# Optimization experiments

Measured on AMD Instinct MI355X. Metric: run time of the kernel, lower is better.

Reference implementation:

```python
import jax, jax.numpy as jnp
import numpy as np

N = 100000
E = 1600000
D = 128


def setup_inputs() -> dict:
    key = jax.random.key(0)
    ks = jax.random.split(key, 9)
    s = 1.0 / np.sqrt(D)
    return {
        "x": jax.random.normal(ks[0], (N, D), dtype=jnp.float32),
        "edge_index": jax.random.randint(ks[1], (2, E), 0, N, dtype=jnp.int64),
        # SAGEConv layer 1: lin_l (neighbor path, with bias), lin_r (root path, no bias)
        "Wl1": jax.random.normal(ks[2], (D, D), dtype=jnp.float32) * s,
        "bl1": jnp.zeros((D,), dtype=jnp.float32),
        "Wr1": jax.random.normal(ks[3], (D, D), dtype=jnp.float32) * s,
        # SAGEConv layer 2
        "Wl2": jax.random.normal(ks[4], (D, D), dtype=jnp.float32) * s,
        "bl2": jnp.zeros((D,), dtype=jnp.float32),
        "Wr2": jax.random.normal(ks[5], (D, D), dtype=jnp.float32) * s,
    }


def _sage_conv(x, src, dst, Wl, bl, Wr):
    # PyG SAGEConv, aggr='mean', root_weight=True:
    #   out = lin_l(mean_{j in N(i)} x_j) + lin_r(x_i)
    msg = x[src]                                              # [E, D] gather
    agg = jax.ops.segment_sum(msg, dst, num_segments=N)       # [N, D]
    cnt = jax.ops.segment_sum(jnp.ones((src.shape[0],), x.dtype), dst, num_segments=N)
    agg = agg / jnp.maximum(cnt, 1.0)[:, None]                # mean aggregation
    return agg @ Wl.T + bl + x @ Wr.T


def reference(x, edge_index, Wl1, bl1, Wr1, Wl2, bl2, Wr2):
    src, dst = edge_index[0], edge_index[1]
    h = jax.nn.relu(_sage_conv(x, src, dst, Wl1, bl1, Wr1))
    out = _sage_conv(h, src, dst, Wl2, bl2, Wr2)
    return out
```

## Files before the change

### kernel.cpp

```cpp
#include <hip/hip_runtime.h>
#include <stdint.h>

#define DN 128
#define NBITS 6
#define BNODES 64
#define HB 2048
#define NSL 64
#define NLOC 256

__host__ __device__ static inline int divup(int a, int b){ return (a+b-1)/b; }

typedef __attribute__((ext_vector_type(8))) short bf16x8;
typedef __attribute__((ext_vector_type(4))) float floatx4;

__device__ __forceinline__ unsigned short f2bf(float f){
  unsigned int x = __float_as_uint(f);
  unsigned int r = x + 0x7fffu + ((x >> 16) & 1u);
  return (unsigned short)(r >> 16);
}
__device__ __forceinline__ unsigned int pack2(unsigned short a, unsigned short b){
  return (unsigned int)a | ((unsigned int)b << 16);
}


__global__ __launch_bounds__(256)
void hist_pass(const int* __restrict__ dst, int* __restrict__ gHist, int E){
  __shared__ int h[NLOC];
  int p = blockIdx.x & 7, s = blockIdx.x >> 3;
  int t = threadIdx.x;
  h[t] = 0;
  __syncthreads();
  int n4 = E >> 2, per4 = divup(n4, NSL);
  int lo = s*per4, hi = min(lo+per4, n4);
  const int4* dst4 = (const int4*)dst;
  for (int i = lo + t; i < hi; i += 256){
    int4 d4 = dst4[i];
    int dd[4] = {d4.x, d4.y, d4.z, d4.w};
    #pragma unroll
    for (int j=0;j<4;j++){
      int b = dd[j] >> NBITS;
      if ((b & 7) == p) atomicAdd(&h[b>>3], 1);
    }
  }
  if (s == NSL-1){
    for (int e = (n4<<2) + t; e < E; e += 256){
      int b = dst[e] >> NBITS;
      if ((b & 7) == p) atomicAdd(&h[b>>3], 1);
    }
  }
  __syncthreads();
  gHist[blockIdx.x*NLOC + t] = h[t];
}

__global__ __launch_bounds__(256)
void scan_offsets(const int* __restrict__ gHist, int* __restrict__ blockOffset,
                  int* __restrict__ bucketTotal){
  int b = blockIdx.x*4 + (threadIdx.x >> 6);
  int k = threadIdx.x & 63;
  int p = b & 7, lb = b >> 3;
  int idx = (k*8 + p)*NLOC + lb;
  int v = gHist[idx];
  int sft = v;
  #pragma unroll
  for (int off=1; off<64; off<<=1){
    int u = __shfl_up(sft, off, 64);
    if (k >= off) sft += u;
  }
  blockOffset[idx] = sft - v;
  if (k == 63) bucketTotal[b] = sft;
}

__global__ __launch_bounds__(256)
void bucket_base(const int* __restrict__ bucketTotal, int* __restrict__ bucketBase){
  __shared__ int s[256];
  int t = threadIdx.x;
  int v[8]; int sum = 0;
  #pragma unroll
  for (int j=0;j<8;j++){ v[j] = bucketTotal[t*8+j]; sum += v[j]; }
  s[t] = sum; __syncthreads();
  for (int off=1; off<256; off<<=1){
    int y = (t>=off)? s[t-off] : 0;
    __syncthreads();
    s[t] += y;
    __syncthreads();
  }
  int excl = s[t] - sum;
  #pragma unroll
  for (int j=0;j<8;j++){ bucketBase[t*8+j] = excl; excl += v[j]; }
  if (t == 255) bucketBase[HB] = excl;
}

__global__ __launch_bounds__(256)
void scatter_pass(const int* __restrict__ src, const int* __restrict__ dst,
                  const int* __restrict__ bucketBase, const int* __restrict__ blockOffset,
                  unsigned int* __restrict__ packed, int E){
  __shared__ int cur[NLOC];
  int p = blockIdx.x & 7, s = blockIdx.x >> 3;
  int t = threadIdx.x;
  cur[t] = bucketBase[(t<<3)|p] + blockOffset[blockIdx.x*NLOC + t];
  __syncthreads();
  int n4 = E >> 2, per4 = divup(n4, NSL);
  int lo = s*per4, hi = min(lo+per4, n4);
  const int4* dst4 = (const int4*)dst;
  const int4* src4 = (const int4*)src;
  for (int i = lo + t; i < hi; i += 256){
    int4 d4 = dst4[i];
    int4 s4 = src4[i];
    int dd[4] = {d4.x, d4.y, d4.z, d4.w};
    int ss[4] = {s4.x, s4.y, s4.z, s4.w};
    #pragma unroll
    for (int j=0;j<4;j++){
      int d = dd[j], b = d >> NBITS;
      if ((b & 7) == p){
        int pos = atomicAdd(&cur[b>>3], 1);
        packed[pos] = (unsigned)ss[j] | ((unsigned)(d & (BNODES-1)) << 17);
      }
    }
  }
  if (s == NSL-1){
    for (int e = (n4<<2) + t; e < E; e += 256){
      int d = dst[e], b = d >> NBITS;
      if ((b & 7) == p){
        int pos = atomicAdd(&cur[b>>3], 1);
        packed[pos] = (unsigned)src[e] | ((unsigned)(d & (BNODES-1)) << 17);
      }
    }
  }
}

__global__ __launch_bounds__(256)
void node_sort(const int* __restrict__ bucketBase, const unsigned int* __restrict__ packed,
               int* __restrict__ csr_src, int* __restrict__ nodeOff, int n){
  __shared__ int cnts[BNODES], offs[BNODES+1], cursor[BNODES];
  int b = blockIdx.x, t = threadIdx.x;
  int beg = bucketBase[b], end = bucketBase[b+1], cnt = end - beg;
  if (t < BNODES) cnts[t] = 0;
  __syncthreads();
  for (int i=t; i<cnt; i+=256) atomicAdd(&cnts[(packed[beg+i]>>17)&63], 1);
  __syncthreads();
  if (t < BNODES){
    int v = cnts[t], sft = v;
    #pragma unroll
    for (int off=1; off<64; off<<=1){
      int u = __shfl_up(sft, off, 64);
      if (t >= off) sft += u;
    }
    offs[t] = sft - v; cursor[t] = sft - v;
    if (t == 63) offs[BNODES] = sft;
  }
  __syncthreads();
  for (int i=t; i<cnt; i+=256){
    unsigned pk = packed[beg+i];
    int nd = (pk>>17)&63;
    int r = atomicAdd(&cursor[nd], 1);
    csr_src[beg + r] = (int)(pk & 0x1FFFFu);
  }
  if (t <= BNODES){
    int node = b*BNODES + t;
    if (node <= n) nodeOff[node] = beg + offs[t];
  }
}


__global__ __launch_bounds__(256)
void convert_x_kernel(const float* __restrict__ src, unsigned short* __restrict__ dst, int count8){
  int i = blockIdx.x*256 + threadIdx.x;
  if (i >= count8) return;
  const float4* s = (const float4*)src + (size_t)i*2;
  float4 a = s[0], b = s[1];
  uint4 o;
  o.x = pack2(f2bf(a.x), f2bf(a.y));
  o.y = pack2(f2bf(a.z), f2bf(a.w));
  o.z = pack2(f2bf(b.x), f2bf(b.y));
  o.w = pack2(f2bf(b.z), f2bf(b.w));
  ((uint4*)dst)[i] = o;
}

__global__ __launch_bounds__(256)
void convert_w_kernel(const float* __restrict__ w0, const float* __restrict__ w1,
                      const float* __restrict__ w2, const float* __restrict__ w3,
                      unsigned short* __restrict__ dst){
  int tid = blockIdx.x*256 + threadIdx.x;
  if (tid >= 8192) return;
  int mat = tid >> 11, off = tid & 2047;
  const float* w = (mat==0)?w0:(mat==1)?w1:(mat==2)?w2:w3;
  const float4* s = (const float4*)w + (size_t)off*2;
  float4 a = s[0], b = s[1];
  uint4 o;
  o.x = pack2(f2bf(a.x), f2bf(a.y));
  o.y = pack2(f2bf(a.z), f2bf(a.w));
  o.z = pack2(f2bf(b.x), f2bf(b.y));
  o.w = pack2(f2bf(b.z), f2bf(b.w));
  ((uint4*)(dst + (size_t)mat*16384))[off] = o;
}

__global__ __launch_bounds__(256)
void aggregate_csr(const unsigned short* __restrict__ xb, const int* __restrict__ nodeOff,
                   const int* __restrict__ csr_src, unsigned short* __restrict__ aggb, int n){
  int g = (blockIdx.x*256 + threadIdx.x) >> 4;
  int l = threadIdx.x & 15;
  if (g >= n) return;
  int beg = nodeOff[g], end = nodeOff[g+1];
  float acc[8] = {0,0,0,0,0,0,0,0};
  #define ACCUM(u) { unsigned int w;                                   \
      w=(u).x; acc[0]+=__uint_as_float(w<<16); acc[1]+=__uint_as_float(w&0xffff0000u); \
      w=(u).y; acc[2]+=__uint_as_float(w<<16); acc[3]+=__uint_as_float(w&0xffff0000u); \
      w=(u).z; acc[4]+=__uint_as_float(w<<16); acc[5]+=__uint_as_float(w&0xffff0000u); \
      w=(u).w; acc[6]+=__uint_as_float(w<<16); acc[7]+=__uint_as_float(w&0xffff0000u); }
  int p = beg;
  for (; p+4 <= end; p += 4){
    int s0 = csr_src[p], s1 = csr_src[p+1], s2 = csr_src[p+2], s3 = csr_src[p+3];
    uint4 u0 = ((const uint4*)(xb + (size_t)s0*DN))[l];
    uint4 u1 = ((const uint4*)(xb + (size_t)s1*DN))[l];
    uint4 u2 = ((const uint4*)(xb + (size_t)s2*DN))[l];
    uint4 u3 = ((const uint4*)(xb + (size_t)s3*DN))[l];
    ACCUM(u0) ACCUM(u1) ACCUM(u2) ACCUM(u3)
  }
  for (; p < end; ++p){
    int s0 = csr_src[p];
    uint4 u0 = ((const uint4*)(xb + (size_t)s0*DN))[l];
    ACCUM(u0)
  }
  #undef ACCUM
  float inv = 1.f / fmaxf((float)(end-beg), 1.f);
  uint4 o;
  o.x = pack2(f2bf(acc[0]*inv), f2bf(acc[1]*inv));
  o.y = pack2(f2bf(acc[2]*inv), f2bf(acc[3]*inv));
  o.z = pack2(f2bf(acc[4]*inv), f2bf(acc[5]*inv));
  o.w = pack2(f2bf(acc[6]*inv), f2bf(acc[7]*inv));
  ((uint4*)(aggb + (size_t)g*DN))[l] = o;
}

template<bool RELU, bool OUT_BF16>
__global__ __launch_bounds__(256)
void gemm_mfma(const unsigned short* __restrict__ A1, const unsigned short* __restrict__ W1b,
               const unsigned short* __restrict__ A2, const unsigned short* __restrict__ W2b,
               const float* __restrict__ bias, void* __restrict__ out,
               int rt_total, int rt_per_block)
{
  int wave = threadIdx.x >> 6;
  int lane = threadIdx.x & 63;
  int m = lane & 15, quad = lane >> 4;

  bf16x8 Bf[2][2][4];
  {
    const unsigned short* Ws[2] = {W1b, W2b};
    #pragma unroll
    for (int c2=0;c2<2;c2++){
      int col = wave*32 + c2*16 + m;
      #pragma unroll
      for (int mat=0;mat<2;mat++){
        const unsigned short* wrow = Ws[mat] + (size_t)col*DN + quad*8;
        #pragma unroll
        for (int kc=0;kc<4;kc++)
          Bf[c2][mat][kc] = *(const bf16x8*)(wrow + kc*32);
      }
    }
  }
  float bv0 = bias[wave*32 + m];
  float bv1 = bias[wave*32 + 16 + m];

  int rt_begin = blockIdx.x * rt_per_block;
  int rt_end = rt_begin + rt_per_block; if (rt_end > rt_total) rt_end = rt_total;

  for (int rt = rt_begin; rt < rt_end; ++rt){
    const unsigned short* a1p = A1 + ((size_t)(rt*16 + m))*DN + quad*8;
    const unsigned short* a2p = A2 + ((size_t)(rt*16 + m))*DN + quad*8;
    bf16x8 Af[2][4];
    #pragma unroll
    for (int kc=0;kc<4;kc++){
      Af[0][kc] = *(const bf16x8*)(a1p + kc*32);
      Af[1][kc] = *(const bf16x8*)(a2p + kc*32);
    }
    __syncthreads();
    floatx4 acc0 = {0.f,0.f,0.f,0.f}, acc1 = {0.f,0.f,0.f,0.f};
    #pragma unroll
    for (int mat=0; mat<2; mat++)
      #pragma unroll
      for (int kc=0; kc<4; kc++){
        acc0 = __builtin_amdgcn_mfma_f32_16x16x32_bf16(Af[mat][kc], Bf[0][mat][kc], acc0, 0,0,0);
        acc1 = __builtin_amdgcn_mfma_f32_16x16x32_bf16(Af[mat][kc], Bf[1][mat][kc], acc1, 0,0,0);
      }
    #pragma unroll
    for (int r=0;r<4;r++){
      int row = rt*16 + quad*4 + r;
      float v0 = acc0[r] + bv0;
      float v1 = acc1[r] + bv1;
      if (RELU){ v0 = fmaxf(v0, 0.f); v1 = fmaxf(v1, 0.f); }
      if (OUT_BF16){
        unsigned short* o = (unsigned short*)out + (size_t)row*DN + wave*32 + m;
        o[0]  = f2bf(v0);
        o[16] = f2bf(v1);
      } else {
        float* o = (float*)out + (size_t)row*DN + wave*32 + m;
        o[0]  = v0;
        o[16] = v1;
      }
    }
  }
}


extern "C" void kernel_launch(void* const* d_in, const int* in_sizes, int n_in,
                              void* d_out, int out_size, void* d_ws, size_t ws_size,
                              hipStream_t stream) {
  const float* x   = (const float*)d_in[0];
  const int*   ei  = (const int*)d_in[1];
  const float* Wl1 = (const float*)d_in[2];
  const float* bl1 = (const float*)d_in[3];
  const float* Wr1 = (const float*)d_in[4];
  const float* Wl2 = (const float*)d_in[5];
  const float* bl2 = (const float*)d_in[6];
  const float* Wr2 = (const float*)d_in[7];

  const int n = in_sizes[0] / DN;
  const int E = in_sizes[1] / 2;
  const int* src = ei;
  const int* dst = ei + E;

  char* ws = (char*)d_ws;
  char* ws_end = ws + ws_size;
  int* gHist       = (int*)ws;  ws += (size_t)NSL*8*NLOC*4;
  int* blockOffset = (int*)ws;  ws += (size_t)NSL*8*NLOC*4;
  int* bucketTotal = (int*)ws;  ws += (size_t)HB*4;
  int* bucketBase  = (int*)ws;  ws += (size_t)(HB+1)*4;
  ws = (char*)(((uintptr_t)ws + 255) & ~(uintptr_t)255);
  unsigned int* packed = (unsigned int*)ws; ws += (size_t)E*4;
  int* csr_src     = (int*)ws;  ws += (size_t)E*4;
  int* nodeOff     = (int*)ws;  ws += (size_t)(n+1)*4;
  ws = (char*)(((uintptr_t)ws + 255) & ~(uintptr_t)255);
  unsigned short* Wb   = (unsigned short*)ws; ws += 4*16384*2;
  unsigned short* xb   = (unsigned short*)ws; ws += (size_t)n*DN*2;
  unsigned short* aggb = (unsigned short*)ws; ws += (size_t)n*DN*2;
  unsigned short* hb = xb;
  if (ws + (size_t)n*DN*2 <= ws_end) { hb = (unsigned short*)ws; ws += (size_t)n*DN*2; }

  unsigned short* Wl1b = Wb;
  unsigned short* Wr1b = Wb + 16384;
  unsigned short* Wl2b = Wb + 2*16384;
  unsigned short* Wr2b = Wb + 3*16384;

  hist_pass   <<<NSL*8, 256,0,stream>>>(dst, gHist, E);
  scan_offsets<<<HB/4,  256,0,stream>>>(gHist, blockOffset, bucketTotal);
  bucket_base <<<1,     256,0,stream>>>(bucketTotal, bucketBase);
  scatter_pass<<<NSL*8, 256,0,stream>>>(src, dst, bucketBase, blockOffset, packed, E);
  node_sort   <<<HB,    256,0,stream>>>(bucketBase, packed, csr_src, nodeOff, n);

  convert_x_kernel<<<divup(n*DN/8,256),256,0,stream>>>(x, xb, n*DN/8);
  convert_w_kernel<<<32,256,0,stream>>>(Wl1, Wr1, Wl2, Wr2, Wb);

  const int rt_total = n / 16;
  const int rt_per_block = 5;
  const int gblocks = divup(rt_total, rt_per_block);
  const int agrid = divup(n*16, 256);

  aggregate_csr<<<agrid,256,0,stream>>>(xb, nodeOff, csr_src, aggb, n);
  gemm_mfma<true, true><<<gblocks,256,0,stream>>>(aggb, Wl1b, xb, Wr1b, bl1, hb, rt_total, rt_per_block);
  aggregate_csr<<<agrid,256,0,stream>>>(hb, nodeOff, csr_src, aggb, n);
  gemm_mfma<false,false><<<gblocks,256,0,stream>>>(aggb, Wl2b, hb, Wr2b, bl2, d_out, rt_total, rt_per_block);
}
```

Measured before the change: 362.9 us.

## Store node features in column slabs for cache-local aggregation gather

Feature matrices are stored as 8 column slabs of 16 bf16 values per node (each slab n*16 elements), so every aggregation block reads only one 3.2MB slab. The gather's working set can then fit in L2/MALL instead of spanning the whole 25MB feature matrix. The GEMM loads A fragments and writes bf16 outputs in the slab layout. In exchange each edge's src index is reread by 8 blocks, and the grid becomes a fixed 512 blocks with a strided node loop.

```diff
diff --git a/kernel.cpp b/kernel.cpp
--- a/kernel.cpp
+++ b/kernel.cpp
@@ -21,6 +21,7 @@
 __device__ __forceinline__ unsigned int pack2(unsigned short a, unsigned short b){
   return (unsigned int)a | ((unsigned int)b << 16);
 }
+
 
 
 __global__ __launch_bounds__(256)
@@ -163,7 +164,8 @@
 
 
 __global__ __launch_bounds__(256)
-void convert_x_kernel(const float* __restrict__ src, unsigned short* __restrict__ dst, int count8){
+void convert_x_kernel(const float* __restrict__ src, unsigned short* __restrict__ dst,
+                      int count8, int n){
   int i = blockIdx.x*256 + threadIdx.x;
   if (i >= count8) return;
   const float4* s = (const float4*)src + (size_t)i*2;
@@ -173,7 +175,9 @@
   o.y = pack2(f2bf(a.z), f2bf(a.w));
   o.z = pack2(f2bf(b.x), f2bf(b.y));
   o.w = pack2(f2bf(b.z), f2bf(b.w));
-  ((uint4*)dst)[i] = o;
+  int row = i >> 4, c8 = i & 15;
+  unsigned short* d = dst + (size_t)(c8>>1)*n*16 + (size_t)row*16 + (c8&1)*8;
+  *(uint4*)d = o;
 }
 
 __global__ __launch_bounds__(256)
@@ -195,40 +199,48 @@
 }
 
 __global__ __launch_bounds__(256)
-void aggregate_csr(const unsigned short* __restrict__ xb, const int* __restrict__ nodeOff,
-                   const int* __restrict__ csr_src, unsigned short* __restrict__ aggb, int n){
-  int g = (blockIdx.x*256 + threadIdx.x) >> 4;
-  int l = threadIdx.x & 15;
-  if (g >= n) return;
-  int beg = nodeOff[g], end = nodeOff[g+1];
-  float acc[8] = {0,0,0,0,0,0,0,0};
+void aggregate_slab(const unsigned short* __restrict__ xs, const int* __restrict__ nodeOff,
+                    const int* __restrict__ csr_src, unsigned short* __restrict__ aggs, int n){
+  int p = blockIdx.x & 7, s = blockIdx.x >> 3;
+  int t = threadIdx.x;
+  int pid = t >> 1, half = t & 1;
+  const unsigned short* slab = xs + (size_t)p*n*16;
+  unsigned short* oslab = aggs + (size_t)p*n*16;
   #define ACCUM(u) { unsigned int w;                                   \
       w=(u).x; acc[0]+=__uint_as_float(w<<16); acc[1]+=__uint_as_float(w&0xffff0000u); \
       w=(u).y; acc[2]+=__uint_as_float(w<<16); acc[3]+=__uint_as_float(w&0xffff0000u); \
       w=(u).z; acc[4]+=__uint_as_float(w<<16); acc[5]+=__uint_as_float(w&0xffff0000u); \
       w=(u).w; acc[6]+=__uint_as_float(w<<16); acc[7]+=__uint_as_float(w&0xffff0000u); }
-  int p = beg;
-  for (; p+4 <= end; p += 4){
-    int s0 = csr_src[p], s1 = csr_src[p+1], s2 = csr_src[p+2], s3 = csr_src[p+3];
-    uint4 u0 = ((const uint4*)(xb + (size_t)s0*DN))[l];
-    uint4 u1 = ((const uint4*)(xb + (size_t)s1*DN))[l];
-    uint4 u2 = ((const uint4*)(xb + (size_t)s2*DN))[l];
-    uint4 u3 = ((const uint4*)(xb + (size_t)s3*DN))[l];
-    ACCUM(u0) ACCUM(u1) ACCUM(u2) ACCUM(u3)
-  }
-  for (; p < end; ++p){
-    int s0 = csr_src[p];
-    uint4 u0 = ((const uint4*)(xb + (size_t)s0*DN))[l];
-    ACCUM(u0)
+  for (int g = s*128 + pid; g < n; g += NSL*128){
+    int beg = nodeOff[g], end = nodeOff[g+1];
+    float acc[8] = {0,0,0,0,0,0,0,0};
+    int e = beg;
+    for (; e+4 <= end; e += 4){
+      int s0 = csr_src[e], s1 = csr_src[e+1], s2 = csr_src[e+2], s3 = csr_src[e+3];
+      uint4 u0 = *(const uint4*)(slab + (size_t)s0*16 + half*8);
+      uint4 u1 = *(const uint4*)(slab + (size_t)s1*16 + half*8);
+      uint4 u2 = *(const uint4*)(slab + (size_t)s2*16 + half*8);
+      uint4 u3 = *(const uint4*)(slab + (size_t)s3*16 + half*8);
+      ACCUM(u0) ACCUM(u1) ACCUM(u2) ACCUM(u3)
+    }
+    for (; e < end; ++e){
+      int s0 = csr_src[e];
+      uint4 u0 = *(const uint4*)(slab + (size_t)s0*16 + half*8);
+      ACCUM(u0)
+    }
+    float inv = 1.f / fmaxf((float)(end-beg), 1.f);
+    uint4 o;
+    o.x = pack2(f2bf(acc[0]*inv), f2bf(acc[1]*inv));
+    o.y = pack2(f2bf(acc[2]*inv), f2bf(acc[3]*inv));
+    o.z = pack2(f2bf(acc[4]*inv), f2bf(acc[5]*inv));
+    o.w = pack2(f2bf(acc[6]*inv), f2bf(acc[7]*inv));
+    *(uint4*)(oslab + (size_t)g*16 + half*8) = o;
   }
   #undef ACCUM
-  float inv = 1.f / fmaxf((float)(end-beg), 1.f);
-  uint4 o;
-  o.x = pack2(f2bf(acc[0]*inv), f2bf(acc[1]*inv));
-  o.y = pack2(f2bf(acc[2]*inv), f2bf(acc[3]*inv));
-  o.z = pack2(f2bf(acc[4]*inv), f2bf(acc[5]*inv));
-  o.w = pack2(f2bf(acc[6]*inv), f2bf(acc[7]*inv));
-  ((uint4*)(aggb + (size_t)g*DN))[l] = o;
+}
+
+__device__ __forceinline__ bf16x8 load_slabA(const unsigned short* base, int n, int row, int c){
+  return *(const bf16x8*)(base + (size_t)(c>>4)*n*16 + (size_t)row*16 + (c&15));
 }
 
 template<bool RELU, bool OUT_BF16>
@@ -236,7 +248,7 @@
 void gemm_mfma(const unsigned short* __restrict__ A1, const unsigned short* __restrict__ W1b,
                const unsigned short* __restrict__ A2, const unsigned short* __restrict__ W2b,
                const float* __restrict__ bias, void* __restrict__ out,
-               int rt_total, int rt_per_block)
+               int rt_total, int rt_per_block, int n)
 {
   int wave = threadIdx.x >> 6;
   int lane = threadIdx.x & 63;
@@ -264,13 +276,13 @@
   int rt_end = rt_begin + rt_per_block; if (rt_end > rt_total) rt_end = rt_total;
 
   for (int rt = rt_begin; rt < rt_end; ++rt){
-    const unsigned short* a1p = A1 + ((size_t)(rt*16 + m))*DN + quad*8;
-    const unsigned short* a2p = A2 + ((size_t)(rt*16 + m))*DN + quad*8;
+    int row0 = rt*16 + m;
     bf16x8 Af[2][4];
     #pragma unroll
     for (int kc=0;kc<4;kc++){
-      Af[0][kc] = *(const bf16x8*)(a1p + kc*32);
-      Af[1][kc] = *(const bf16x8*)(a2p + kc*32);
+      int c = kc*32 + quad*8;
+      Af[0][kc] = load_slabA(A1, n, row0, c);
+      Af[1][kc] = load_slabA(A2, n, row0, c);
     }
     __syncthreads();
     floatx4 acc0 = {0.f,0.f,0.f,0.f}, acc1 = {0.f,0.f,0.f,0.f};
@@ -288,9 +300,9 @@
       float v1 = acc1[r] + bv1;
       if (RELU){ v0 = fmaxf(v0, 0.f); v1 = fmaxf(v1, 0.f); }
       if (OUT_BF16){
-        unsigned short* o = (unsigned short*)out + (size_t)row*DN + wave*32 + m;
-        o[0]  = f2bf(v0);
-        o[16] = f2bf(v1);
+        unsigned short* o = (unsigned short*)out;
+        o[(size_t)(2*wave  )*n*16 + (size_t)row*16 + m] = f2bf(v0);
+        o[(size_t)(2*wave+1)*n*16 + (size_t)row*16 + m] = f2bf(v1);
       } else {
         float* o = (float*)out + (size_t)row*DN + wave*32 + m;
         o[0]  = v0;
@@ -346,16 +358,15 @@
   scatter_pass<<<NSL*8, 256,0,stream>>>(src, dst, bucketBase, blockOffset, packed, E);
   node_sort   <<<HB,    256,0,stream>>>(bucketBase, packed, csr_src, nodeOff, n);
 
-  convert_x_kernel<<<divup(n*DN/8,256),256,0,stream>>>(x, xb, n*DN/8);
+  convert_x_kernel<<<divup(n*DN/8,256),256,0,stream>>>(x, xb, n*DN/8, n);
   convert_w_kernel<<<32,256,0,stream>>>(Wl1, Wr1, Wl2, Wr2, Wb);
 
   const int rt_total = n / 16;
   const int rt_per_block = 5;
   const int gblocks = divup(rt_total, rt_per_block);
-  const int agrid = divup(n*16, 256);
-
-  aggregate_csr<<<agrid,256,0,stream>>>(xb, nodeOff, csr_src, aggb, n);
-  gemm_mfma<true, true><<<gblocks,256,0,stream>>>(aggb, Wl1b, xb, Wr1b, bl1, hb, rt_total, rt_per_block);
-  aggregate_csr<<<agrid,256,0,stream>>>(hb, nodeOff, csr_src, aggb, n);
-  gemm_mfma<false,false><<<gblocks,256,0,stream>>>(aggb, Wl2b, hb, Wr2b, bl2, d_out, rt_total, rt_per_block);
-}
+
+  aggregate_slab<<<NSL*8,256,0,stream>>>(xb, nodeOff, csr_src, aggb, n);
+  gemm_mfma<true, true><<<gblocks,256,0,stream>>>(aggb, Wl1b, xb, Wr1b, bl1, hb, rt_total, rt_per_block, n);
+  aggregate_slab<<<NSL*8,256,0,stream>>>(hb, nodeOff, csr_src, aggb, n);
+  gemm_mfma<false,false><<<gblocks,256,0,stream>>>(aggb, Wl2b, hb, Wr2b, bl2, d_out, rt_total, rt_per_block, n);
+}
```

Result: slower. 419.9 us (+15.7%).
